# Performance work log

Measured on AMD Instinct MI355X. Metric: run time of the kernel, lower is better.

Reference implementation:

```python
import jax, jax.numpy as jnp
import numpy as np

# ---- module constants (from __init__ defaults) ----
OUTPUT_BIT = 8
NBIT = 16            # self.N, fixed-point fraction bits for piecewise coeffs
EXP_BITWIDTH = 16
SEGMENTS = 16
DEGREE = 2


def _fit_pieces(x_np, s):
    """Replicates _compute_integer_coefficients (host-side, no_grad numpy path).

    Fits per-segment degree-2 polynomials to the IBERT integer-exp curve over the
    observed range of (x_int - rowmax) * s, then converts to integer fixed-point
    coefficients with N fraction bits.
    """
    x_int = np.floor(x_np.astype(np.float64) / s)
    x_int = x_int - x_int.max(axis=-1, keepdims=True)
    x_float = x_int * s
    x_lo = float(np.floor(x_float.min()))
    x_hi = min(float(np.ceil(x_float.max())), 0.0)
    xs = np.linspace(x_lo, x_hi, 10000, dtype=np.float32)
    xs_int = np.floor(xs / np.float32(s))
    # IBERT integer exp: exp(x) ~ 2^(-q) * poly(r), x = q*x0 + r, x0 = -ln2
    c0 = 0.35815147
    c1 = 0.96963238 / c0
    c2 = 1.0 / c0
    x0, n = -0.6931, 30
    x0_int = np.floor(np.float32(x0 / s))
    xi = np.maximum(xs_int, n * x0_int)
    q = np.floor(xi / x0_int)
    r = xi - x0_int * q
    b_int = np.floor(np.float32(c1 / s))
    c_int = np.floor(np.float32(c2 / s ** 2))
    z = r * (r + b_int) + c_int
    exp_int = np.clip(np.floor(z * 2.0 ** (n - q)), 0, None)
    ys = (exp_int * ((c0 * s ** 2) / 2.0 ** n)).astype(np.float32)
    bounds = np.linspace(x_lo, x_hi, SEGMENTS + 1, dtype=np.float32)
    lo_l, hi_l, cf_l = [], [], []
    for lo, hi in zip(bounds[:-1], bounds[1:]):
        m = (xs >= lo) & (xs <= hi)
        cf = np.polyfit(xs[m].astype(np.float64), ys[m].astype(np.float64), DEGREE).astype(np.float32)
        lo_l.append(np.floor(lo / s))
        hi_l.append(np.floor(hi / s))
        deg = len(cf) - 1
        cf_l.append([np.floor(np.float32(c) * s ** (deg - i) * 2.0 ** NBIT) for i, c in enumerate(cf)])
    return (np.asarray(lo_l, np.float32), np.asarray(hi_l, np.float32), np.asarray(cf_l, np.float32))


def setup_inputs() -> dict:
    key = jax.random.key(0)
    x = jax.random.normal(key, (4, 12, 1024, 1024), dtype=jnp.float32)  # [B,H,S,S] attn logits
    s = 0.01  # realistic 8-bit logit quantization scale
    lo_b, hi_b, coeffs = _fit_pieces(np.asarray(x), s)
    return {
        "x": x,
        "scaling_factor": jnp.asarray(s, dtype=jnp.float32),
        "lo_bounds": jnp.asarray(lo_b),
        "hi_bounds": jnp.asarray(hi_b),
        "coeffs": jnp.asarray(coeffs),  # [SEGMENTS, DEGREE+1], highest power first
    }


def reference(x, scaling_factor, lo_bounds, hi_bounds, coeffs):
    # quantize and shift so rowwise max -> 0 (hi_bounds kept for signature parity;
    # segments are contiguous so lo_bounds alone determines segment membership,
    # with ties at boundaries resolved to the higher segment as in the torch loop)
    x_int = jnp.floor(x / scaling_factor)
    x_int = x_int - jnp.max(x_int, axis=-1, keepdims=True)

    # piecewise polynomial int-exp: pick segment, Horner-evaluate integer coeffs
    seg = jnp.clip(jnp.searchsorted(lo_bounds, x_int, side="right") - 1, 0, SEGMENTS - 1)
    c = coeffs[seg]  # [..., DEGREE+1]
    r = c[..., 0]
    for i in range(1, DEGREE + 1):
        r = r * x_int + c[..., i]
    exp_int = jnp.maximum(r, 0.0)

    # renormalize exp to EXP_BITWIDTH bits, then integer softmax
    exp_int = jnp.floor(exp_int / 2.0 ** (30 - EXP_BITWIDTH + 1))
    exp_sum = jnp.maximum(jnp.sum(exp_int, axis=-1, keepdims=True), 1.0)
    factor = jnp.floor(2.0 ** 32 / exp_sum)
    softmax_int = jnp.floor(exp_int * factor / 2.0 ** (32 - OUTPUT_BIT + 1))

    softmax_float = jax.nn.softmax(x, axis=-1)
    s_out = jnp.float32(2.0 / 2.0 ** OUTPUT_BIT)
    si = softmax_int * s_out
    # straight-through combine, then re-quantize to the output grid
    output = jax.lax.stop_gradient(si) + (softmax_float - jax.lax.stop_gradient(softmax_float))
    output = s_out * jnp.floor(output / s_out)
    return output, jnp.array([s_out], dtype=x.dtype)
```

## Files before the change

### kernel.cpp

```cpp
#include <hip/hip_runtime.h>


constexpr int ROW = 1024;
constexpr int WPB = 4;
constexpr int TSIZE = 2048;

typedef float f32x4 __attribute__((ext_vector_type(4)));

__global__ __launch_bounds__(256) void intsoftmax_kernel(
    const float* __restrict__ x,
    const float* __restrict__ s_ptr,
    const float* __restrict__ lo_bounds,
    const float* __restrict__ coeffs,
    float* __restrict__ out,
    int rows)
{
    __shared__ float4 sc[16];
    __shared__ float slo[16];
    __shared__ float etab[TSIZE];

    const int tid = threadIdx.x;
    if (tid < 16) {
        sc[tid] = make_float4(coeffs[tid * 3 + 0],
                              coeffs[tid * 3 + 1],
                              coeffs[tid * 3 + 2], 0.0f);
        slo[tid] = lo_bounds[tid];
    }
    __syncthreads();

    for (int i = tid; i < TSIZE; i += 256) {
        const float xv = (float)(i - (TSIZE - 1));
        int seg = 0;
#pragma unroll
        for (int j = 1; j < 16; ++j) seg += (xv >= slo[j]) ? 1 : 0;
        const float4 c = sc[seg];
        float r = __fadd_rn(__fmul_rn(c.x, xv), c.y);
        r = __fadd_rn(__fmul_rn(r, xv), c.z);
        etab[i] = floorf(fmaxf(r, 0.0f) * (1.0f / 32768.0f));
    }
    __syncthreads();

    if (blockIdx.x == 0 && tid == 0) {
        out[(size_t)rows * ROW] = 0.0078125f;
    }

    const float s = s_ptr[0];
    const float rcp = __fdiv_rn(1.0f, s);

    const int wave = tid >> 6;
    const int lane = tid & 63;
    const long long row = (long long)blockIdx.x * WPB + wave;
    if (row >= rows) return;

    const float4* __restrict__ xr = (const float4*)(x + row * (long long)ROW);

    float xi[16];
#pragma unroll
    for (int c4 = 0; c4 < 4; ++c4) {
        const float4 v = xr[c4 * 64 + lane];
        {
            const float q0 = __fmul_rn(v.x, rcp);
            xi[c4*4+0] = floorf(__builtin_fmaf(__builtin_fmaf(-s, q0, v.x), rcp, q0));
        }
        {
            const float q0 = __fmul_rn(v.y, rcp);
            xi[c4*4+1] = floorf(__builtin_fmaf(__builtin_fmaf(-s, q0, v.y), rcp, q0));
        }
        {
            const float q0 = __fmul_rn(v.z, rcp);
            xi[c4*4+2] = floorf(__builtin_fmaf(__builtin_fmaf(-s, q0, v.z), rcp, q0));
        }
        {
            const float q0 = __fmul_rn(v.w, rcp);
            xi[c4*4+3] = floorf(__builtin_fmaf(__builtin_fmaf(-s, q0, v.w), rcp, q0));
        }
    }

    float m = xi[0];
#pragma unroll
    for (int k = 1; k < 16; ++k) m = fmaxf(m, xi[k]);
#pragma unroll
    for (int off = 32; off >= 1; off >>= 1)
        m = fmaxf(m, __shfl_xor(m, off, 64));

    int idx[16];
    int imin = 0;
#pragma unroll
    for (int k = 0; k < 16; ++k) {
        idx[k] = (int)(xi[k] - m) + (TSIZE - 1);
        imin = min(imin, idx[k]);
    }

    float e[16];
    float psum = 0.0f;
    if (__builtin_expect(!__any(imin < 0), 1)) {
#pragma unroll
        for (int k = 0; k < 16; ++k) {
            e[k] = etab[idx[k]];
            psum += e[k];
        }
    } else {
#pragma unroll
        for (int k = 0; k < 16; ++k) {
            const float xv = xi[k] - m;
            int seg = 0;
#pragma unroll
            for (int j = 1; j < 16; ++j) seg += (xv >= slo[j]) ? 1 : 0;
            const float4 c = sc[seg];
            float r = __fadd_rn(__fmul_rn(c.x, xv), c.y);
            r = __fadd_rn(__fmul_rn(r, xv), c.z);
            e[k] = floorf(fmaxf(r, 0.0f) * (1.0f / 32768.0f));
            psum += e[k];
        }
    }

    float sum = psum;
#pragma unroll
    for (int off = 32; off >= 1; off >>= 1)
        sum += __shfl_xor(sum, off, 64);

    const float factor = floorf(__fdiv_rn(4294967296.0f, fmaxf(sum, 1.0f)));

    f32x4* const orow_v = (f32x4*)(out + row * (long long)ROW);
#pragma unroll
    for (int c4 = 0; c4 < 4; ++c4) {
        f32x4 o;
        o.x = floorf(__fmul_rn(e[c4*4+0], factor) * (1.0f/33554432.0f)) * 0.0078125f;
        o.y = floorf(__fmul_rn(e[c4*4+1], factor) * (1.0f/33554432.0f)) * 0.0078125f;
        o.z = floorf(__fmul_rn(e[c4*4+2], factor) * (1.0f/33554432.0f)) * 0.0078125f;
        o.w = floorf(__fmul_rn(e[c4*4+3], factor) * (1.0f/33554432.0f)) * 0.0078125f;
        __builtin_nontemporal_store(o, orow_v + c4 * 64 + lane);
    }
}

extern "C" void kernel_launch(void* const* d_in, const int* in_sizes, int n_in,
                              void* d_out, int out_size, void* d_ws, size_t ws_size,
                              hipStream_t stream) {
    const float* x      = (const float*)d_in[0];
    const float* s      = (const float*)d_in[1];
    const float* lo     = (const float*)d_in[2];
    const float* coeffs = (const float*)d_in[4];
    float* out = (float*)d_out;

    const int n = in_sizes[0];
    const int rows = n / ROW;
    const int blocks = (rows + WPB - 1) / WPB;

    hipLaunchKernelGGL(intsoftmax_kernel, dim3(blocks), dim3(256), 0, stream,
                       x, s, lo, coeffs, out, rows);
}
```

Baseline: 59.49 us.

## Precompute exp lookup table once in workspace and copy it into LDS per block

Adds a small pre-kernel that evaluates the 2048-entry piecewise-polynomial exp table into the workspace buffer. The main kernel then fills its LDS table with two vector loads per thread instead of recomputing every entry with segment search and Horner evaluation in each of the 12288 blocks. It also folds the max subtraction into a per-row integer base and pre-scales the normalization factor to remove one multiply per element. The cost is an extra kernel launch and a global-memory read of the table in each block; when no workspace is available, the kernel falls back to building the table itself.

```diff
diff --git a/kernel.cpp b/kernel.cpp
--- a/kernel.cpp
+++ b/kernel.cpp
@@ -7,36 +7,63 @@
 
 typedef float f32x4 __attribute__((ext_vector_type(4)));
 
+__device__ __forceinline__ float eval_e(float xv,
+                                        const float* __restrict__ lo,
+                                        const float4* __restrict__ cf) {
+    int seg = 0;
+#pragma unroll
+    for (int j = 1; j < 16; ++j) seg += (xv >= lo[j]) ? 1 : 0;
+    const float4 c = cf[seg];
+    float r = __fadd_rn(__fmul_rn(c.x, xv), c.y);
+    r = __fadd_rn(__fmul_rn(r, xv), c.z);
+    return floorf(fmaxf(r, 0.0f) * (1.0f / 32768.0f));
+}
+
+__global__ __launch_bounds__(256) void build_etab_kernel(
+    const float* __restrict__ lo_bounds,
+    const float* __restrict__ coeffs,
+    float* __restrict__ gtab)
+{
+    const int i = blockIdx.x * 256 + threadIdx.x;
+    if (i >= TSIZE) return;
+    float lo[16];
+    float4 cf[16];
+#pragma unroll
+    for (int j = 0; j < 16; ++j) {
+        lo[j] = lo_bounds[j];
+        cf[j] = make_float4(coeffs[j*3+0], coeffs[j*3+1], coeffs[j*3+2], 0.0f);
+    }
+    gtab[i] = eval_e((float)(i - (TSIZE - 1)), lo, cf);
+}
+
+template <bool LOAD_TAB>
 __global__ __launch_bounds__(256) void intsoftmax_kernel(
     const float* __restrict__ x,
     const float* __restrict__ s_ptr,
     const float* __restrict__ lo_bounds,
     const float* __restrict__ coeffs,
+    const float* __restrict__ gtab,
     float* __restrict__ out,
     int rows)
 {
-    __shared__ float4 sc[16];
-    __shared__ float slo[16];
     __shared__ float etab[TSIZE];
+    const int tid = threadIdx.x;
 
-    const int tid = threadIdx.x;
-    if (tid < 16) {
-        sc[tid] = make_float4(coeffs[tid * 3 + 0],
-                              coeffs[tid * 3 + 1],
-                              coeffs[tid * 3 + 2], 0.0f);
-        slo[tid] = lo_bounds[tid];
-    }
-    __syncthreads();
-
-    for (int i = tid; i < TSIZE; i += 256) {
-        const float xv = (float)(i - (TSIZE - 1));
-        int seg = 0;
+    if (LOAD_TAB) {
+        const f32x4* __restrict__ gt = (const f32x4*)gtab;
+        f32x4* lt = (f32x4*)etab;
+        lt[tid]       = gt[tid];
+        lt[tid + 256] = gt[tid + 256];
+    } else {
+        float lo[16];
+        float4 cf[16];
 #pragma unroll
-        for (int j = 1; j < 16; ++j) seg += (xv >= slo[j]) ? 1 : 0;
-        const float4 c = sc[seg];
-        float r = __fadd_rn(__fmul_rn(c.x, xv), c.y);
-        r = __fadd_rn(__fmul_rn(r, xv), c.z);
-        etab[i] = floorf(fmaxf(r, 0.0f) * (1.0f / 32768.0f));
+        for (int j = 0; j < 16; ++j) {
+            lo[j] = lo_bounds[j];
+            cf[j] = make_float4(coeffs[j*3+0], coeffs[j*3+1], coeffs[j*3+2], 0.0f);
+        }
+        for (int i = tid; i < TSIZE; i += 256)
+            etab[i] = eval_e((float)(i - (TSIZE - 1)), lo, cf);
     }
     __syncthreads();
 
@@ -83,11 +110,12 @@
     for (int off = 32; off >= 1; off >>= 1)
         m = fmaxf(m, __shfl_xor(m, off, 64));
 
+    const int base = (TSIZE - 1) - (int)m;
     int idx[16];
-    int imin = 0;
+    int imin = TSIZE;
 #pragma unroll
     for (int k = 0; k < 16; ++k) {
-        idx[k] = (int)(xi[k] - m) + (TSIZE - 1);
+        idx[k] = (int)xi[k] + base;
         imin = min(imin, idx[k]);
     }
 
@@ -100,16 +128,16 @@
             psum += e[k];
         }
     } else {
+        float lo[16];
+        float4 cf[16];
+#pragma unroll
+        for (int j = 0; j < 16; ++j) {
+            lo[j] = lo_bounds[j];
+            cf[j] = make_float4(coeffs[j*3+0], coeffs[j*3+1], coeffs[j*3+2], 0.0f);
+        }
 #pragma unroll
         for (int k = 0; k < 16; ++k) {
-            const float xv = xi[k] - m;
-            int seg = 0;
-#pragma unroll
-            for (int j = 1; j < 16; ++j) seg += (xv >= slo[j]) ? 1 : 0;
-            const float4 c = sc[seg];
-            float r = __fadd_rn(__fmul_rn(c.x, xv), c.y);
-            r = __fadd_rn(__fmul_rn(r, xv), c.z);
-            e[k] = floorf(fmaxf(r, 0.0f) * (1.0f / 32768.0f));
+            e[k] = eval_e(xi[k] - m, lo, cf);
             psum += e[k];
         }
     }
@@ -120,15 +148,16 @@
         sum += __shfl_xor(sum, off, 64);
 
     const float factor = floorf(__fdiv_rn(4294967296.0f, fmaxf(sum, 1.0f)));
+    const float factor25 = factor * (1.0f / 33554432.0f);
 
     f32x4* const orow_v = (f32x4*)(out + row * (long long)ROW);
 #pragma unroll
     for (int c4 = 0; c4 < 4; ++c4) {
         f32x4 o;
-        o.x = floorf(__fmul_rn(e[c4*4+0], factor) * (1.0f/33554432.0f)) * 0.0078125f;
-        o.y = floorf(__fmul_rn(e[c4*4+1], factor) * (1.0f/33554432.0f)) * 0.0078125f;
-        o.z = floorf(__fmul_rn(e[c4*4+2], factor) * (1.0f/33554432.0f)) * 0.0078125f;
-        o.w = floorf(__fmul_rn(e[c4*4+3], factor) * (1.0f/33554432.0f)) * 0.0078125f;
+        o.x = floorf(__fmul_rn(e[c4*4+0], factor25)) * 0.0078125f;
+        o.y = floorf(__fmul_rn(e[c4*4+1], factor25)) * 0.0078125f;
+        o.z = floorf(__fmul_rn(e[c4*4+2], factor25)) * 0.0078125f;
+        o.w = floorf(__fmul_rn(e[c4*4+3], factor25)) * 0.0078125f;
         __builtin_nontemporal_store(o, orow_v + c4 * 64 + lane);
     }
 }
@@ -146,6 +175,14 @@
     const int rows = n / ROW;
     const int blocks = (rows + WPB - 1) / WPB;
 
-    hipLaunchKernelGGL(intsoftmax_kernel, dim3(blocks), dim3(256), 0, stream,
-                       x, s, lo, coeffs, out, rows);
+    if (ws_size >= TSIZE * sizeof(float)) {
+        float* gtab = (float*)d_ws;
+        hipLaunchKernelGGL(build_etab_kernel, dim3(TSIZE / 256), dim3(256), 0,
+                           stream, lo, coeffs, gtab);
+        hipLaunchKernelGGL(intsoftmax_kernel<true>, dim3(blocks), dim3(256), 0,
+                           stream, x, s, lo, coeffs, gtab, out, rows);
+    } else {
+        hipLaunchKernelGGL(intsoftmax_kernel<false>, dim3(blocks), dim3(256), 0,
+                           stream, x, s, lo, coeffs, (const float*)nullptr, out, rows);
+    }
 }
```

After: 59.88 us. About the same (+0.7%).
